# Kernel tuning notes

Hardware: AMD Instinct MI355X
Metric: run time of the kernel (lower is better)

The kernel has to match this reference:

```python
import jax, jax.numpy as jnp
import numpy as np

EPS = 1e-5
N_HEADS = 12


def _layernorm(x, scale, shift):
    mean = jnp.mean(x, axis=-1, keepdims=True)
    var = jnp.mean((x - mean) ** 2, axis=-1, keepdims=True)
    return scale * (x - mean) / jnp.sqrt(var + EPS) + shift


def setup_inputs() -> dict:
    key = jax.random.key(0)
    ks = jax.random.split(key, 8)
    B, L, D = 4, 1024, 768
    inp = {
        "x": jax.random.normal(ks[0], (B, L, D), jnp.float32),
        "Wq": jax.random.normal(ks[1], (D, D), jnp.float32) * 0.02,
        "Wk": jax.random.normal(ks[2], (D, D), jnp.float32) * 0.02,
        "Wv": jax.random.normal(ks[3], (D, D), jnp.float32) * 0.02,
        "Wo": jax.random.normal(ks[4], (D, D), jnp.float32) * 0.02,
        "bo": jnp.zeros((D,), jnp.float32),
        "scale1": jnp.ones((D,), jnp.float32),
        "shift1": jnp.zeros((D,), jnp.float32),
        "scale2": jnp.ones((D,), jnp.float32),
        "shift2": jnp.zeros((D,), jnp.float32),
        "centers": jax.random.normal(ks[5], (D, D), jnp.float32) * 0.1,  # [num_kernels=D, D]
        "lengthscale": jnp.ones((D,), jnp.float32),
        "Wf": jax.random.normal(ks[6], (D, D), jnp.float32) * 0.02,  # [num_kernels, D]
        "bf": jnp.zeros((D,), jnp.float32),
    }
    return inp


def reference(x, Wq, Wk, Wv, Wo, bo, scale1, shift1, scale2, shift2,
              centers, lengthscale, Wf, bf):
    B, L, D = x.shape
    H = N_HEADS
    hd = D // H

    # --- pre-norm causal MHA + residual ---
    h = _layernorm(x, scale1, shift1)
    q = (h @ Wq).reshape(B, L, H, hd).transpose(0, 2, 1, 3)  # [B,H,L,hd]
    k = (h @ Wk).reshape(B, L, H, hd).transpose(0, 2, 1, 3)
    v = (h @ Wv).reshape(B, L, H, hd).transpose(0, 2, 1, 3)

    scores = jnp.einsum("bhqd,bhkd->bhqk", q, k) / jnp.sqrt(jnp.float32(hd))
    causal = jnp.tril(jnp.ones((L, L), bool))
    scores = jnp.where(causal, scores, -jnp.inf)
    attn = jax.nn.softmax(scores, axis=-1)
    ctx = jnp.einsum("bhqk,bhkd->bhqd", attn, v).transpose(0, 2, 1, 3).reshape(B, L, D)
    x = x + (ctx @ Wo + bo)

    # --- pre-norm RBF-kernel FFN + residual ---
    h = _layernorm(x, scale2, shift2)
    hf = (h / lengthscale).reshape(B * L, D)          # ARD scaling
    cf = centers / lengthscale                        # [K, D]
    sq = (jnp.sum(hf * hf, -1)[:, None]
          + jnp.sum(cf * cf, -1)[None, :]
          - 2.0 * hf @ cf.T)
    K = jnp.exp(-0.5 * jnp.maximum(sq, 0.0))          # [B*L, K]
    ff = (K @ Wf + bf).reshape(B, L, D)
    return x + ff
```

## Files before the change

kernel.cpp:

```cpp
#include <hip/hip_runtime.h>

#define EPS_LN 1e-5f

constexpr int Dm   = 768;
constexpr int Bb   = 4;
constexpr int Ls   = 1024;
constexpr int Hh   = 12;
constexpr int HD   = 64;
constexpr int ROWS = Bb * Ls;
constexpr size_t S = (size_t)ROWS * Dm;
constexpr size_t WSZ = (size_t)Dm * Dm;

typedef __attribute__((ext_vector_type(8))) short bf16x8;
typedef __attribute__((ext_vector_type(4))) float f32x4;
typedef const __attribute__((address_space(1))) unsigned int* gas_p;
typedef __attribute__((address_space(3))) unsigned int* las_p;

__device__ __forceinline__ unsigned short f2bf(float f) {
  unsigned int u = __float_as_uint(f);
  u += 0x7fffu + ((u >> 16) & 1u);
  return (unsigned short)(u >> 16);
}
__device__ __forceinline__ void gl_lds16(const unsigned short* g, unsigned short* l) {
  __builtin_amdgcn_global_load_lds((gas_p)g, (las_p)l, 16, 0, 0);
}

__global__ void __launch_bounds__(256) prep_kernel(
    const float* __restrict__ W0, const float* __restrict__ W1,
    const float* __restrict__ W2, const float* __restrict__ W3,
    const float* __restrict__ W4, unsigned short* __restrict__ wtBase,
    const float* __restrict__ centers, const float* __restrict__ ls,
    unsigned short* __restrict__ cb, float* __restrict__ cn,
    const float* __restrict__ x, const float* __restrict__ scale,
    const float* __restrict__ shift, unsigned short* __restrict__ hb)
{
  __shared__ float smem[64 * 65];
  int bx = blockIdx.x, t = threadIdx.x;
  if (bx < 720) {
    int w = bx / 144, rem = bx - w * 144;
    int ky = rem / 12, nx = rem - ky * 12;
    const float* W = w == 0 ? W0 : w == 1 ? W1 : w == 2 ? W2 : w == 3 ? W3 : W4;
    unsigned short* WT = wtBase + (size_t)w * WSZ;
    int k0 = ky * 64, n0 = nx * 64;
    int c = t & 63, r4 = t >> 6;
    #pragma unroll
    for (int p = 0; p < 16; p++) {
      int r = p * 4 + r4;
      smem[r * 65 + c] = W[(size_t)(k0 + r) * Dm + n0 + c];
    }
    __syncthreads();
    #pragma unroll
    for (int p = 0; p < 16; p++) {
      int r = p * 4 + r4;
      WT[(size_t)(n0 + r) * Dm + k0 + c] = f2bf(smem[c * 65 + r]);
    }
  } else if (bx < 1488) {
    int j = bx - 720;
    float s = 0.f;
    #pragma unroll
    for (int i = 0; i < 3; i++) {
      int k = t + 256 * i;
      float c = centers[(size_t)j * Dm + k] / ls[k];
      cb[(size_t)j * Dm + k] = f2bf(c);
      s += c * c;
    }
    smem[t] = s; __syncthreads();
    for (int o = 128; o > 0; o >>= 1) { if (t < o) smem[t] += smem[t + o]; __syncthreads(); }
    if (t == 0) cn[j] = smem[0];
  } else {
    int lane = t & 63;
    int row = (bx - 1488) * 4 + (t >> 6);
    size_t base = (size_t)row * Dm;
    float4 v[3];
    #pragma unroll
    for (int j = 0; j < 3; j++)
      v[j] = *(const float4*)&x[base + 4 * (lane + 64 * j)];
    float sum = 0.f;
    #pragma unroll
    for (int j = 0; j < 3; j++) sum += v[j].x + v[j].y + v[j].z + v[j].w;
    #pragma unroll
    for (int m = 1; m < 64; m <<= 1) sum += __shfl_xor(sum, m);
    float mean = sum * (1.0f / Dm);
    float4 d[3];
    float vs = 0.f;
    #pragma unroll
    for (int j = 0; j < 3; j++) {
      d[j].x = v[j].x - mean; d[j].y = v[j].y - mean;
      d[j].z = v[j].z - mean; d[j].w = v[j].w - mean;
      vs += d[j].x*d[j].x + d[j].y*d[j].y + d[j].z*d[j].z + d[j].w*d[j].w;
    }
    #pragma unroll
    for (int m = 1; m < 64; m <<= 1) vs += __shfl_xor(vs, m);
    float rstd = rsqrtf(vs * (1.0f / Dm) + EPS_LN);
    #pragma unroll
    for (int j = 0; j < 3; j++) {
      int c4 = 4 * (lane + 64 * j);
      float4 sc = *(const float4*)&scale[c4];
      float4 sh = *(const float4*)&shift[c4];
      ushort4 o4;
      o4.x = f2bf(sc.x * d[j].x * rstd + sh.x);
      o4.y = f2bf(sc.y * d[j].y * rstd + sh.y);
      o4.z = f2bf(sc.z * d[j].z * rstd + sh.z);
      o4.w = f2bf(sc.w * d[j].w * rstd + sh.w);
      *(ushort4*)&hb[base + c4] = o4;
    }
  }
}

__global__ void __launch_bounds__(256) ln2_kernel(
    const float* __restrict__ xin, const float* __restrict__ scale,
    const float* __restrict__ shift, const float* __restrict__ ls,
    unsigned short* __restrict__ o, float* __restrict__ hn)
{
  int lane = threadIdx.x & 63;
  int row = blockIdx.x * 4 + (threadIdx.x >> 6);
  size_t base = (size_t)row * Dm;
  float4 v[3];
  #pragma unroll
  for (int j = 0; j < 3; j++)
    v[j] = *(const float4*)&xin[base + 4 * (lane + 64 * j)];
  float sum = 0.f;
  #pragma unroll
  for (int j = 0; j < 3; j++) sum += v[j].x + v[j].y + v[j].z + v[j].w;
  #pragma unroll
  for (int m = 1; m < 64; m <<= 1) sum += __shfl_xor(sum, m);
  float mean = sum * (1.0f / Dm);
  float4 d[3];
  float vs = 0.f;
  #pragma unroll
  for (int j = 0; j < 3; j++) {
    d[j].x = v[j].x - mean; d[j].y = v[j].y - mean;
    d[j].z = v[j].z - mean; d[j].w = v[j].w - mean;
    vs += d[j].x*d[j].x + d[j].y*d[j].y + d[j].z*d[j].z + d[j].w*d[j].w;
  }
  #pragma unroll
  for (int m = 1; m < 64; m <<= 1) vs += __shfl_xor(vs, m);
  float rstd = rsqrtf(vs * (1.0f / Dm) + EPS_LN);
  float hsum = 0.f;
  #pragma unroll
  for (int j = 0; j < 3; j++) {
    int c4 = 4 * (lane + 64 * j);
    float4 sc = *(const float4*)&scale[c4];
    float4 sh = *(const float4*)&shift[c4];
    float4 lv = *(const float4*)&ls[c4];
    float4 hv;
    hv.x = (sc.x * d[j].x * rstd + sh.x) / lv.x;
    hv.y = (sc.y * d[j].y * rstd + sh.y) / lv.y;
    hv.z = (sc.z * d[j].z * rstd + sh.z) / lv.z;
    hv.w = (sc.w * d[j].w * rstd + sh.w) / lv.w;
    ushort4 o4;
    o4.x = f2bf(hv.x); o4.y = f2bf(hv.y); o4.z = f2bf(hv.z); o4.w = f2bf(hv.w);
    *(ushort4*)&o[base + c4] = o4;
    hsum += hv.x*hv.x + hv.y*hv.y + hv.z*hv.z + hv.w*hv.w;
  }
  #pragma unroll
  for (int m = 1; m < 64; m <<= 1) hsum += __shfl_xor(hsum, m);
  if (lane == 0) hn[row] = hsum;
}

__global__ void __launch_bounds__(256) gemm_qkv(
    const unsigned short* __restrict__ Abf,
    const unsigned short* __restrict__ wqT,
    const unsigned short* __restrict__ wkT,
    const unsigned short* __restrict__ wvT,
    unsigned short* __restrict__ qb,
    unsigned short* __restrict__ kb,
    unsigned short* __restrict__ vbt)
{
  int m0 = blockIdx.y * 64, n0 = blockIdx.x * 64;
  __shared__ unsigned short sm[4096 + 3 * 4096];
  int tid = threadIdx.x;
  int lane = tid & 63, wave = tid >> 6;
  int quad = lane >> 4, l15 = lane & 15;
  int wr = (wave >> 1) << 5, wc = (wave & 1) << 5;

  f32x4 acc[3][2][2];
  #pragma unroll
  for (int w = 0; w < 3; w++)
    #pragma unroll
    for (int i = 0; i < 2; i++)
      #pragma unroll
      for (int j = 0; j < 2; j++) acc[w][i][j] = (f32x4){0.f, 0.f, 0.f, 0.f};

  const unsigned short* gA = Abf + (size_t)(m0 + (tid >> 2)) * Dm + ((tid & 3) << 3);
  size_t bOff = (size_t)(n0 + (tid >> 2)) * Dm + ((tid & 3) << 3);
  const unsigned short* gB[3] = { wqT + bOff, wkT + bOff, wvT + bOff };

  union Frag { bf16x8 v; ushort4 h[2]; };

  for (int k0 = 0; k0 < Dm; k0 += 64) {
    gl_lds16(gA + k0,      &sm[tid * 8]);
    gl_lds16(gA + k0 + 32, &sm[2048 + tid * 8]);
    #pragma unroll
    for (int w = 0; w < 3; w++) {
      gl_lds16(gB[w] + k0,      &sm[4096 + w * 4096 + tid * 8]);
      gl_lds16(gB[w] + k0 + 32, &sm[4096 + w * 4096 + 2048 + tid * 8]);
    }
    __syncthreads();
    Frag af[2][2];
    #pragma unroll
    for (int kc = 0; kc < 2; kc++)
      #pragma unroll
      for (int mi = 0; mi < 2; mi++)
        af[kc][mi].v = *(const bf16x8*)&sm[kc * 2048 + (wr + mi * 16 + l15) * 32 + quad * 8];
    #pragma unroll
    for (int w = 0; w < 3; w++)
      #pragma unroll
      for (int kc = 0; kc < 2; kc++)
        #pragma unroll
        for (int ni = 0; ni < 2; ni++) {
          Frag bf;
          bf.v = *(const bf16x8*)&sm[4096 + w * 4096 + kc * 2048 + (wc + ni * 16 + l15) * 32 + quad * 8];
          #pragma unroll
          for (int mi = 0; mi < 2; mi++)
            acc[w][mi][ni] = __builtin_amdgcn_mfma_f32_16x16x32_bf16(
                af[kc][mi].v, bf.v, acc[w][mi][ni], 0, 0, 0);
        }
    __syncthreads();
  }

  #pragma unroll
  for (int w = 0; w < 2; w++) {
    unsigned short* ob = w ? kb : qb;
    #pragma unroll
    for (int mi = 0; mi < 2; mi++)
      #pragma unroll
      for (int ni = 0; ni < 2; ni++)
        #pragma unroll
        for (int rg = 0; rg < 4; rg++) {
          int gr = m0 + wr + mi * 16 + quad * 4 + rg;
          int gc = n0 + wc + ni * 16 + l15;
          ob[(size_t)gr * Dm + gc] = f2bf(acc[w][mi][ni][rg]);
        }
  }
  #pragma unroll
  for (int mi = 0; mi < 2; mi++)
    #pragma unroll
    for (int ni = 0; ni < 2; ni++)
      #pragma unroll
      for (int rg = 0; rg < 4; rg++) {
        int rl = wr + mi * 16 + quad * 4 + rg;
        int cl = wc + ni * 16 + l15;
        sm[cl * 72 + rl] = f2bf(acc[2][mi][ni][rg]);
      }
  __syncthreads();
  {
    int d = tid >> 2, c0 = (tid & 3) * 16;
    int b_ = m0 >> 10, keybase = m0 & 1023;
    unsigned short* dst = vbt + ((size_t)((blockIdx.x * 4 + b_) * 64 + d)) * 1024 + keybase + c0;
    #pragma unroll
    for (int i = 0; i < 16; i += 4)
      *(ushort4*)(dst + i) = *(const ushort4*)&sm[d * 72 + c0 + i];
  }
}

template<int MODE>
__global__ void __launch_bounds__(256) gemm64(
    const unsigned short* __restrict__ Abf,
    const unsigned short* __restrict__ BT,
    unsigned short* __restrict__ o0,
    float* __restrict__ outF,
    const float* __restrict__ residF,
    const float* __restrict__ biasF,
    const float* __restrict__ hn,
    const float* __restrict__ cn)
{
  __shared__ unsigned short Asm[2][2048];
  __shared__ unsigned short Bsm[2][2048];
  int tid = threadIdx.x;
  int m0 = blockIdx.y * 64, n0 = blockIdx.x * 64;

  if (MODE >= 2) {
    __shared__ float r2[256];
    float mn = 1e30f;
    for (int i = tid; i < ROWS; i += 256) mn = fminf(mn, hn[i]);
    r2[tid] = mn; __syncthreads();
    for (int o = 128; o > 0; o >>= 1) { if (tid < o) r2[tid] = fminf(r2[tid], r2[tid + o]); __syncthreads(); }
    float hmin = r2[0];
    __syncthreads();
    float mx = 0.f;
    for (int i = tid; i < Dm; i += 256) mx = fmaxf(mx, cn[i]);
    r2[tid] = mx; __syncthreads();
    for (int o = 128; o > 0; o >>= 1) { if (tid < o) r2[tid] = fmaxf(r2[tid], r2[tid + o]); __syncthreads(); }
    float cmax = r2[0];
    float a = sqrtf(hmin), bq = sqrtf(cmax);
    bool allz = (a > bq) && ((a - bq) * (a - bq) > 300.0f);
    if (allz) {
      if (MODE == 2) return;
      int r = m0 + (tid >> 2), c0 = n0 + (tid & 3) * 16;
      size_t idx = (size_t)r * Dm + c0;
      #pragma unroll
      for (int i = 0; i < 16; i += 4) {
        float4 xv = *(const float4*)(residF + idx + i);
        float4 ov;
        ov.x = xv.x + biasF[c0 + i + 0];
        ov.y = xv.y + biasF[c0 + i + 1];
        ov.z = xv.z + biasF[c0 + i + 2];
        ov.w = xv.w + biasF[c0 + i + 3];
        *(float4*)(outF + idx + i) = ov;
      }
      return;
    }
    __syncthreads();
  }

  int lane = tid & 63, wave = tid >> 6;
  int quad = lane >> 4, l15 = lane & 15;
  int wr = (wave >> 1) << 5, wc = (wave & 1) << 5;

  f32x4 acc[2][2];
  #pragma unroll
  for (int i = 0; i < 2; i++)
    #pragma unroll
    for (int j = 0; j < 2; j++) acc[i][j] = (f32x4){0.f, 0.f, 0.f, 0.f};

  const unsigned short* gA = Abf + (size_t)(m0 + (tid >> 2)) * Dm + ((tid & 3) << 3);
  const unsigned short* gB = BT  + (size_t)(n0 + (tid >> 2)) * Dm + ((tid & 3) << 3);

  union Frag { bf16x8 v; ushort4 h[2]; };

  for (int k0 = 0; k0 < Dm; k0 += 64) {
    gl_lds16(gA + k0,      &Asm[0][tid * 8]);
    gl_lds16(gA + k0 + 32, &Asm[1][tid * 8]);
    gl_lds16(gB + k0,      &Bsm[0][tid * 8]);
    gl_lds16(gB + k0 + 32, &Bsm[1][tid * 8]);
    __syncthreads();
    #pragma unroll
    for (int kc = 0; kc < 2; kc++) {
      Frag af[2], bfb[2];
      #pragma unroll
      for (int i = 0; i < 2; i++) {
        af[i].v  = *(const bf16x8*)&Asm[kc][(wr + i * 16 + l15) * 32 + quad * 8];
        bfb[i].v = *(const bf16x8*)&Bsm[kc][(wc + i * 16 + l15) * 32 + quad * 8];
      }
      #pragma unroll
      for (int mi = 0; mi < 2; mi++)
        #pragma unroll
        for (int ni = 0; ni < 2; ni++)
          acc[mi][ni] = __builtin_amdgcn_mfma_f32_16x16x32_bf16(
              af[mi].v, bfb[ni].v, acc[mi][ni], 0, 0, 0);
    }
    __syncthreads();
  }

  #pragma unroll
  for (int mi = 0; mi < 2; mi++)
    #pragma unroll
    for (int ni = 0; ni < 2; ni++)
      #pragma unroll
      for (int rg = 0; rg < 4; rg++) {
        int gr = m0 + wr + mi * 16 + quad * 4 + rg;
        int gc = n0 + wc + ni * 16 + l15;
        size_t idx = (size_t)gr * Dm + gc;
        float v = acc[mi][ni][rg];
        if (MODE == 2) {
          float sq = fmaxf(hn[gr] + cn[gc] - 2.0f * v, 0.f);
          o0[idx] = f2bf(__expf(-0.5f * sq));
        } else {
          outF[idx] = residF[idx] + v + biasF[gc];
        }
      }
}

__global__ void __launch_bounds__(256) attn_flash(
    const unsigned short* __restrict__ q,
    const unsigned short* __restrict__ k,
    const unsigned short* __restrict__ vbt,
    unsigned short* __restrict__ ctx)
{
  int bx = blockIdx.x;
  int qt = (bx & 1) ? (15 - (bx >> 1)) : (bx >> 1);
  int h  = blockIdx.y;
  int b  = blockIdx.z;
  int tid = threadIdx.x;
  int lane = tid & 63, wave = tid >> 6;
  int quad = lane >> 4, l15 = lane & 15;

  __shared__ unsigned short Ks[2][2048];
  __shared__ unsigned short Vt[2][2048];
  __shared__ unsigned short QP[4608];

  size_t baseQK = (size_t)(b * Ls) * Dm + h * HD;
  const unsigned short* gVt = vbt + (size_t)((h * 4 + b) * 64 + (tid >> 2)) * 1024 + ((tid & 3) << 3);

  {
    const unsigned short* gQ = q + baseQK + (size_t)(qt * 64 + (tid >> 2)) * Dm + ((tid & 3) << 3);
    gl_lds16(gQ,      &QP[tid * 8]);
    gl_lds16(gQ + 32, &QP[2048 + tid * 8]);
  }
  __syncthreads();

  union Frag { bf16x8 v; ushort4 h[2]; };
  Frag afq[2];
  #pragma unroll
  for (int kc = 0; kc < 2; kc++)
    afq[kc].v = *(const bf16x8*)&QP[kc * 2048 + (wave * 16 + l15) * 32 + quad * 8];

  f32x4 O[4];
  #pragma unroll
  for (int nj = 0; nj < 4; nj++) O[nj] = (f32x4){0.f, 0.f, 0.f, 0.f};
  float lsum[4] = {0.f, 0.f, 0.f, 0.f};

  const unsigned short* gK = k + baseQK + (size_t)(tid >> 2) * Dm + ((tid & 3) << 3);

  for (int kt = 0; kt <= qt; kt++) {
    gl_lds16(gK + (size_t)(kt * 64) * Dm,      &Ks[0][tid * 8]);
    gl_lds16(gK + (size_t)(kt * 64) * Dm + 32, &Ks[1][tid * 8]);
    gl_lds16(gVt + kt * 64,      &Vt[0][tid * 8]);
    gl_lds16(gVt + kt * 64 + 32, &Vt[1][tid * 8]);
    __syncthreads();

    f32x4 sacc[4];
    #pragma unroll
    for (int ni = 0; ni < 4; ni++) {
      sacc[ni] = (f32x4){0.f, 0.f, 0.f, 0.f};
      #pragma unroll
      for (int kc = 0; kc < 2; kc++) {
        Frag bk;
        bk.v = *(const bf16x8*)&Ks[kc][(ni * 16 + l15) * 32 + quad * 8];
        sacc[ni] = __builtin_amdgcn_mfma_f32_16x16x32_bf16(afq[kc].v, bk.v, sacc[ni], 0, 0, 0);
      }
    }

    if (kt == qt) {
      #pragma unroll
      for (int ni = 0; ni < 4; ni++)
        #pragma unroll
        for (int rg = 0; rg < 4; rg++) {
          int rowl = wave * 16 + quad * 4 + rg;
          int coll = ni * 16 + l15;
          if (coll > rowl) sacc[ni][rg] = -1e30f;
        }
    }

    unsigned short (*Ps)[72] = (unsigned short(*)[72])QP;
    #pragma unroll
    for (int ni = 0; ni < 4; ni++)
      #pragma unroll
      for (int rg = 0; rg < 4; rg++) {
        float p = __expf(sacc[ni][rg] * 0.125f);
        lsum[rg] += p;
        Ps[wave * 16 + quad * 4 + rg][ni * 16 + l15] = f2bf(p);
      }

    Frag ap[2];
    #pragma unroll
    for (int kc = 0; kc < 2; kc++)
      ap[kc].v = *(const bf16x8*)&Ps[wave * 16 + l15][kc * 32 + quad * 8];

    #pragma unroll
    for (int nj = 0; nj < 4; nj++)
      #pragma unroll
      for (int kc = 0; kc < 2; kc++) {
        Frag bv;
        bv.v = *(const bf16x8*)&Vt[kc][(nj * 16 + l15) * 32 + quad * 8];
        O[nj] = __builtin_amdgcn_mfma_f32_16x16x32_bf16(ap[kc].v, bv.v, O[nj], 0, 0, 0);
      }
    __syncthreads();
  }

  float linv[4];
  #pragma unroll
  for (int rg = 0; rg < 4; rg++) {
    float l = lsum[rg];
    #pragma unroll
    for (int m = 1; m < 16; m <<= 1) l += __shfl_xor(l, m, 16);
    linv[rg] = 1.0f / l;
  }
  #pragma unroll
  for (int nj = 0; nj < 4; nj++)
    #pragma unroll
    for (int rg = 0; rg < 4; rg++) {
      int row = qt * 64 + wave * 16 + quad * 4 + rg;
      int col = nj * 16 + l15;
      ctx[baseQK + (size_t)row * Dm + col] = f2bf(O[nj][rg] * linv[rg]);
    }
}

extern "C" void kernel_launch(void* const* d_in, const int* in_sizes, int n_in,
                              void* d_out, int out_size, void* d_ws, size_t ws_size,
                              hipStream_t stream)
{
  const float* x      = (const float*)d_in[0];
  const float* Wq     = (const float*)d_in[1];
  const float* Wk     = (const float*)d_in[2];
  const float* Wv     = (const float*)d_in[3];
  const float* Wo     = (const float*)d_in[4];
  const float* bo     = (const float*)d_in[5];
  const float* scale1 = (const float*)d_in[6];
  const float* shift1 = (const float*)d_in[7];
  const float* scale2 = (const float*)d_in[8];
  const float* shift2 = (const float*)d_in[9];
  const float* centers= (const float*)d_in[10];
  const float* lsp    = (const float*)d_in[11];
  const float* Wf     = (const float*)d_in[12];
  const float* bfv    = (const float*)d_in[13];
  float* out = (float*)d_out;

  unsigned short* wsu = (unsigned short*)d_ws;
  unsigned short* wqT = wsu;
  unsigned short* wkT = wsu + WSZ;
  unsigned short* wvT = wsu + 2 * WSZ;
  unsigned short* woT = wsu + 3 * WSZ;
  unsigned short* wfT = wsu + 4 * WSZ;
  unsigned short* cb  = wsu + 5 * WSZ;
  unsigned short* bufA = wsu + 6 * WSZ;
  unsigned short* bufB = bufA + S;
  unsigned short* hb  = bufA;
  unsigned short* qb  = bufB;
  unsigned short* kb  = bufB + S;
  unsigned short* vbt = bufB + 2 * S;
  unsigned short* ctx = bufA;
  float* x1f          = (float*)bufB;
  unsigned short* hf  = bufB + 2 * S;
  unsigned short* Km  = bufA;
  float* hn = (float*)(bufB + 3 * S);
  float* cn = hn + ROWS;

  dim3 gg(Dm / 64, ROWS / 64);

  prep_kernel<<<2512, 256, 0, stream>>>(Wq, Wk, Wv, Wo, Wf, wsu,
                                        centers, lsp, cb, cn,
                                        x, scale1, shift1, hb);
  gemm_qkv<<<dim3(12, 64), 256, 0, stream>>>(hb, wqT, wkT, wvT, qb, kb, vbt);
  attn_flash<<<dim3(Ls / 64, Hh, Bb), 256, 0, stream>>>(qb, kb, vbt, ctx);
  gemm64<1><<<gg, 256, 0, stream>>>(ctx, woT, nullptr, x1f, x, bo, nullptr, nullptr);
  ln2_kernel<<<ROWS / 4, 256, 0, stream>>>(x1f, scale2, shift2, lsp, hf, hn);
  gemm64<2><<<gg, 256, 0, stream>>>(hf, cb, Km, nullptr, nullptr, nullptr, hn, cn);
  gemm64<3><<<gg, 256, 0, stream>>>(Km, wfT, nullptr, out, x1f, bfv, hn, cn);
}
```

Before: 186.9 us.

## Double-buffer K/V tiles in flash attention to prefetch next tile

Turns the K and V shared-memory tiles into two buffers and issues the global-to-LDS loads for tile kt+1 before computing on tile kt. Partial vmcnt waits and raw s_barrier calls replace the per-iteration __syncthreads, so load latency can overlap with the MFMA work. The cost is doubled LDS for K/V, which may reduce occupancy, plus fragile hand-written wait counts and barriers.

```diff
diff --git a/kernel.cpp b/kernel.cpp
--- a/kernel.cpp
+++ b/kernel.cpp
@@ -376,8 +376,8 @@
   int lane = tid & 63, wave = tid >> 6;
   int quad = lane >> 4, l15 = lane & 15;
 
-  __shared__ unsigned short Ks[2][2048];
-  __shared__ unsigned short Vt[2][2048];
+  __shared__ unsigned short Ks[2][2][2048];
+  __shared__ unsigned short Vt[2][2][2048];
   __shared__ unsigned short QP[4608];
 
   size_t baseQK = (size_t)(b * Ls) * Dm + h * HD;
@@ -395,6 +395,7 @@
   #pragma unroll
   for (int kc = 0; kc < 2; kc++)
     afq[kc].v = *(const bf16x8*)&QP[kc * 2048 + (wave * 16 + l15) * 32 + quad * 8];
+  asm volatile("s_waitcnt lgkmcnt(0)" ::: "memory");
 
   f32x4 O[4];
   #pragma unroll
@@ -403,12 +404,27 @@
 
   const unsigned short* gK = k + baseQK + (size_t)(tid >> 2) * Dm + ((tid & 3) << 3);
 
+  gl_lds16(gK,      &Ks[0][0][tid * 8]);
+  gl_lds16(gK + 32, &Ks[0][1][tid * 8]);
+  gl_lds16(gVt,      &Vt[0][0][tid * 8]);
+  gl_lds16(gVt + 32, &Vt[0][1][tid * 8]);
+
   for (int kt = 0; kt <= qt; kt++) {
-    gl_lds16(gK + (size_t)(kt * 64) * Dm,      &Ks[0][tid * 8]);
-    gl_lds16(gK + (size_t)(kt * 64) * Dm + 32, &Ks[1][tid * 8]);
-    gl_lds16(gVt + kt * 64,      &Vt[0][tid * 8]);
-    gl_lds16(gVt + kt * 64 + 32, &Vt[1][tid * 8]);
-    __syncthreads();
+    int cur = kt & 1;
+    asm volatile("s_waitcnt lgkmcnt(0)" ::: "memory");
+    __builtin_amdgcn_s_barrier();
+    if (kt < qt) {
+      int nxt = cur ^ 1;
+      gl_lds16(gK + (size_t)((kt + 1) * 64) * Dm,      &Ks[nxt][0][tid * 8]);
+      gl_lds16(gK + (size_t)((kt + 1) * 64) * Dm + 32, &Ks[nxt][1][tid * 8]);
+      gl_lds16(gVt + (kt + 1) * 64,      &Vt[nxt][0][tid * 8]);
+      gl_lds16(gVt + (kt + 1) * 64 + 32, &Vt[nxt][1][tid * 8]);
+      asm volatile("s_waitcnt vmcnt(4)" ::: "memory");
+    } else {
+      asm volatile("s_waitcnt vmcnt(0)" ::: "memory");
+    }
+    __builtin_amdgcn_s_barrier();
+    __builtin_amdgcn_sched_barrier(0);
 
     f32x4 sacc[4];
     #pragma unroll
@@ -417,7 +433,7 @@
       #pragma unroll
       for (int kc = 0; kc < 2; kc++) {
         Frag bk;
-        bk.v = *(const bf16x8*)&Ks[kc][(ni * 16 + l15) * 32 + quad * 8];
+        bk.v = *(const bf16x8*)&Ks[cur][kc][(ni * 16 + l15) * 32 + quad * 8];
         sacc[ni] = __builtin_amdgcn_mfma_f32_16x16x32_bf16(afq[kc].v, bk.v, sacc[ni], 0, 0, 0);
       }
     }
@@ -453,10 +469,9 @@
       #pragma unroll
       for (int kc = 0; kc < 2; kc++) {
         Frag bv;
-        bv.v = *(const bf16x8*)&Vt[kc][(nj * 16 + l15) * 32 + quad * 8];
+        bv.v = *(const bf16x8*)&Vt[cur][kc][(nj * 16 + l15) * 32 + quad * 8];
         O[nj] = __builtin_amdgcn_mfma_f32_16x16x32_bf16(ap[kc].v, bv.v, O[nj], 0, 0, 0);
       }
-    __syncthreads();
   }
 
   float linv[4];
```

After: 185.6 us. Within noise of the previous version (-0.7%).
